# Performance work log

Hardware: AMD Instinct MI355X
Metric: run time of the kernel (lower is better)

Reference implementation:

```python
import jax, jax.numpy as jnp
import numpy as np

L, H, S, HID, E, TOPK = 2, 8, 1024, 512, 8, 2
FFN = 2 * HID
EPS = 1e-5


def setup_inputs() -> dict:
    key = jax.random.key(0)
    ks = jax.random.split(key, 20)
    B = 4
    sc = 0.02
    inp = {
        'x': jax.random.normal(ks[0], (B, S, HID), jnp.float32),
        'encoder_output': jax.random.normal(ks[1], (B, S, HID), jnp.float32),
        # two attentions per layer -> axis 1 of size 2 (0: masked self-attn, 1: cross-attn)
        'attn_wq': jax.random.normal(ks[2], (L, 2, HID, H * HID), jnp.float32) * sc,
        'attn_bq': jnp.zeros((L, 2, H * HID), jnp.float32),
        'attn_wk': jax.random.normal(ks[3], (L, 2, HID, H * HID), jnp.float32) * sc,
        'attn_bk': jnp.zeros((L, 2, H * HID), jnp.float32),
        'attn_wv': jax.random.normal(ks[4], (L, 2, HID, H * HID), jnp.float32) * sc,
        'attn_bv': jnp.zeros((L, 2, H * HID), jnp.float32),
        'attn_wo': jax.random.normal(ks[5], (L, 2, H * HID, HID), jnp.float32) * sc,
        'attn_bo': jnp.zeros((L, 2, HID), jnp.float32),
        'gate_w': jax.random.normal(ks[6], (L, HID, E), jnp.float32) * sc,
        'gate_b': jnp.zeros((L, E), jnp.float32),
        'exp_w1': jax.random.normal(ks[7], (L, E, HID, FFN), jnp.float32) * sc,
        'exp_b1': jnp.zeros((L, E, FFN), jnp.float32),
        'exp_w2': jax.random.normal(ks[8], (L, E, FFN, HID), jnp.float32) * sc,
        'exp_b2': jnp.zeros((L, E, HID), jnp.float32),
        'ln_g': jnp.ones((L, 3, HID), jnp.float32),
        'ln_b': jnp.zeros((L, 3, HID), jnp.float32),
    }
    return inp


def _layernorm(x, g, b):
    m = jnp.mean(x, -1, keepdims=True)
    v = jnp.mean(jnp.square(x - m), -1, keepdims=True)
    return g * (x - m) * jax.lax.rsqrt(v + EPS) + b


def _mha(q_in, k_in, v_in, wq, bq, wk, bk, wv, bv, wo, bo, masked):
    B = q_in.shape[0]
    # torch .view(-1, H, S, h) on [B, S, H*h]: raw memory reshape (faithful quirk)
    q = (q_in @ wq + bq).reshape(B, H, S, HID)
    k = (k_in @ wk + bk).reshape(B, H, S, HID)
    v = (v_in @ wv + bv).reshape(B, H, S, HID)
    scores = jnp.einsum('bhqd,bhkd->bhqk', q, k)  # d_k=1 -> scale = 1.0
    if masked:
        causal = jnp.triu(jnp.ones((S, S), jnp.float32), k=1)
        scores = jnp.where(causal == 1, -jnp.inf, scores)
    attn = jax.nn.softmax(scores, axis=-1)  # dropout off (eval)
    out = jnp.einsum('bhqk,bhkd->bhqd', attn, v)
    out = out.transpose(0, 2, 1, 3).reshape(B, S, H * HID)
    return out @ wo + bo


def _moe(x, gw, gb, w1, b1, w2, b2):
    gate = jax.nn.softmax(x @ gw + gb, axis=-1)  # [B,S,E]
    topw, topi = jax.lax.top_k(gate, TOPK)
    topw = topw / jnp.sum(topw, -1, keepdims=True)
    # faithful bug: the torch loop overwrites, so only k = TOPK-1 survives
    sel = topi[..., TOPK - 1]  # [B,S]
    wsel = topw[..., TOPK - 1]  # [B,S]
    y = jnp.zeros_like(x)
    for e in range(E):
        he = jax.nn.relu(x @ w1[e] + b1[e]) @ w2[e] + b2[e]
        y = y + jnp.where((sel == e)[..., None], he, 0.0)
    return y * wsel[..., None]


def reference(x, encoder_output, attn_wq, attn_bq, attn_wk, attn_bk, attn_wv,
              attn_bv, attn_wo, attn_bo, gate_w, gate_b, exp_w1, exp_b1,
              exp_w2, exp_b2, ln_g, ln_b):
    for l in range(L):
        a = _mha(x, x, x,
                 attn_wq[l, 0], attn_bq[l, 0], attn_wk[l, 0], attn_bk[l, 0],
                 attn_wv[l, 0], attn_bv[l, 0], attn_wo[l, 0], attn_bo[l, 0],
                 masked=True)
        x = _layernorm(a + x, ln_g[l, 0], ln_b[l, 0])
        # cross-attn: query & key from encoder, values from x (faithful to source)
        a2 = _mha(encoder_output, encoder_output, x,
                  attn_wq[l, 1], attn_bq[l, 1], attn_wk[l, 1], attn_bk[l, 1],
                  attn_wv[l, 1], attn_bv[l, 1], attn_wo[l, 1], attn_bo[l, 1],
                  masked=False)
        x = _layernorm(x + a2, ln_g[l, 1], ln_b[l, 1])
        f = _moe(x, gate_w[l], gate_b[l], exp_w1[l], exp_b1[l], exp_w2[l], exp_b2[l])
        x = _layernorm(x + f, ln_g[l, 2], ln_b[l, 2])
    return x
```

## Files before the change

kernel.cpp:

```cpp
#include <hip/hip_runtime.h>
#include <math.h>


typedef unsigned short bf16_t;
typedef __attribute__((ext_vector_type(8))) short s16x8;
typedef __attribute__((ext_vector_type(8))) unsigned short u16x8;
typedef __attribute__((ext_vector_type(4))) float f32x4;

__device__ __forceinline__ float bf2f(bf16_t u) {
    union { unsigned int i; float f; } v; v.i = ((unsigned int)u) << 16; return v.f;
}
__device__ __forceinline__ bf16_t f2bf(float f) {
    union { float f; unsigned int i; } v; v.f = f;
    unsigned int x = v.i;
    return (bf16_t)((x + 0x7fffu + ((x >> 16) & 1u)) >> 16);
}
__device__ __forceinline__ bf16_t bfhi_trunc(float x, float& rem) {
    union { float f; unsigned u; } v; v.f = x;
    unsigned hu = v.u & 0xFFFF0000u;
    union { unsigned u; float f; } h; h.u = hu;
    rem = x - h.f;
    return (bf16_t)(hu >> 16);
}
__device__ __forceinline__ void split_rne(float x, bf16_t& hi, bf16_t& lo) {
    bf16_t h = f2bf(x);
    float hf = bf2f(h);
    lo = f2bf(x - hf);
    hi = h;
}

__device__ __forceinline__ float waveReduceSum(float x) {
    x += __shfl_xor(x, 1);  x += __shfl_xor(x, 2);  x += __shfl_xor(x, 4);
    x += __shfl_xor(x, 8);  x += __shfl_xor(x, 16); x += __shfl_xor(x, 32);
    return x;
}
__device__ __forceinline__ float waveReduceMax(float x) {
    x = fmaxf(x, __shfl_xor(x, 1));  x = fmaxf(x, __shfl_xor(x, 2));
    x = fmaxf(x, __shfl_xor(x, 4));  x = fmaxf(x, __shfl_xor(x, 8));
    x = fmaxf(x, __shfl_xor(x, 16)); x = fmaxf(x, __shfl_xor(x, 32));
    return x;
}

__global__ void probe_kernel(const unsigned int* __restrict__ lng_u32,
                             int* __restrict__ flag)
{
    if (threadIdx.x == 0 && blockIdx.x == 0)
        *flag = (lng_u32[0] == 0x3F803F80u) ? 1 : 0;
}


__device__ __forceinline__ void stage_f32_row(const float* __restrict__ src,
                                              char* rowp, int h, int r)
{
    float xx[16];
    *(float4*)(xx + 0)  = *(const float4*)(src + 0);
    *(float4*)(xx + 4)  = *(const float4*)(src + 4);
    *(float4*)(xx + 8)  = *(const float4*)(src + 8);
    *(float4*)(xx + 12) = *(const float4*)(src + 12);
    u16x8 h0, h1, l0, l1;
#pragma unroll
    for (int i = 0; i < 8; i++) {
        float r0, r1;
        h0[i] = bfhi_trunc(xx[i], r0);      l0[i] = f2bf(r0);
        h1[i] = bfhi_trunc(xx[8 + i], r1);  l1[i] = f2bf(r1);
    }
    const int sw = (r & 7) << 4;
    *(u16x8*)(rowp + ((32 * h + 0)  ^ sw)) = h0;
    *(u16x8*)(rowp + ((32 * h + 16) ^ sw)) = h1;
    *(u16x8*)(rowp + ((64 + 32 * h + 0)  ^ sw)) = l0;
    *(u16x8*)(rowp + ((64 + 32 * h + 16) ^ sw)) = l1;
}

__device__ __forceinline__ void stage_bf16_row(const bf16_t* __restrict__ src,
                                               char* rowp, int h, int r)
{
    u16x8 v0 = *(const u16x8*)(src);
    u16x8 v1 = *(const u16x8*)(src + 8);
    const int sw = (r & 7) << 4;
    *(u16x8*)(rowp + ((32 * h + 0)  ^ sw)) = v0;
    *(u16x8*)(rowp + ((32 * h + 16) ^ sw)) = v1;
}

__device__ __forceinline__ void stage_pair_row(const bf16_t* __restrict__ hi,
                                               const bf16_t* __restrict__ lo,
                                               char* rowp, int h, int r)
{
    u16x8 h0 = *(const u16x8*)(hi);
    u16x8 h1 = *(const u16x8*)(hi + 8);
    u16x8 l0 = *(const u16x8*)(lo);
    u16x8 l1 = *(const u16x8*)(lo + 8);
    const int sw = (r & 7) << 4;
    *(u16x8*)(rowp + ((32 * h + 0)  ^ sw)) = h0;
    *(u16x8*)(rowp + ((32 * h + 16) ^ sw)) = h1;
    *(u16x8*)(rowp + ((64 + 32 * h + 0)  ^ sw)) = l0;
    *(u16x8*)(rowp + ((64 + 32 * h + 16) ^ sw)) = l1;
}

__device__ __forceinline__ void stage_wnn_f32(const float* __restrict__ src,
                                              int ldb, ushort (*Bs)[64],
                                              int kp2, int n8)
{
    float a0[8], a1[8];
    *(float4*)(a0 + 0) = *(const float4*)(src);
    *(float4*)(a0 + 4) = *(const float4*)(src + 4);
    *(float4*)(a1 + 0) = *(const float4*)(src + ldb);
    *(float4*)(a1 + 4) = *(const float4*)(src + ldb + 4);
#pragma unroll
    for (int j = 0; j < 8; j++) {
        int rr = n8 + j;
        float q0, q1;
        bf16_t h0 = bfhi_trunc(a0[j], q0);
        bf16_t h1 = bfhi_trunc(a1[j], q1);
        unsigned vh = (unsigned)h0 | ((unsigned)h1 << 16);
        unsigned vl = (unsigned)f2bf(q0) | ((unsigned)f2bf(q1) << 16);
        char* rp = (char*)&Bs[rr][0];
        int sw = (rr & 7) << 4;
        *(unsigned*)(rp + ((2 * kp2) ^ sw)) = vh;
        *(unsigned*)(rp + ((64 + 2 * kp2) ^ sw)) = vl;
    }
}

__device__ __forceinline__ void stage_wnn_bf16(const bf16_t* __restrict__ src,
                                               int ldb, ushort (*Bs)[64],
                                               int kp2, int n8, int base)
{
    u16x8 r0 = *(const u16x8*)(src);
    u16x8 r1 = *(const u16x8*)(src + ldb);
#pragma unroll
    for (int j = 0; j < 8; j++) {
        int rr = n8 + j;
        unsigned v = (unsigned)(unsigned short)r0[j] |
                     ((unsigned)(unsigned short)r1[j] << 16);
        *(unsigned*)((char*)&Bs[rr][0] + ((base + 2 * kp2) ^ ((rr & 7) << 4))) = v;
    }
}

template<bool NT, bool RELU, bool GATHER, bool SCALE, bool OUTP>
__device__ __forceinline__
void mgemm_body(int am, const float* __restrict__ aF,
                const bf16_t* __restrict__ aH, const bf16_t* __restrict__ aL,
                int bm, const float* __restrict__ bF,
                const bf16_t* __restrict__ bH, const bf16_t* __restrict__ bL,
                const float* __restrict__ biasF, const bf16_t* __restrict__ biasH,
                const bool bf, const bool hasb,
                float* __restrict__ Cp, bf16_t* __restrict__ CpH, long cplane,
                int lda, int ldb, int ldc,
                int Meff, const int* __restrict__ gl,
                const float* __restrict__ scalev,
                int kBeg, int kEnd, int m0, int n0)
{
    __shared__ __align__(16) ushort As[128][64];
    __shared__ __align__(16) ushort Bs[128][64];

    const int t   = threadIdx.x;
    const int sr  = t >> 1;
    const int sh  = t & 1;
    const int kp2 = (t & 15) * 2;
    const int n8  = (t >> 4) * 8;

    int agr = m0 + sr;
    if (GATHER) agr = gl[(m0 + sr < Meff) ? (m0 + sr) : (Meff - 1)];

    const int lane = t & 63;
    const int wv = t >> 6;
    const int wr = wv >> 1, wc = wv & 1;
    const int lr = lane & 15, kg = lane >> 4;

    int aoffH[4], aoffL[4], boffH[4], boffL[4];
#pragma unroll
    for (int i = 0; i < 4; i++) {
        int ra = wr * 64 + i * 16 + lr;
        int sa = (ra & 7) << 4;
        aoffH[i] = ra * 128 + ((kg * 16) ^ sa);
        aoffL[i] = ra * 128 + ((64 + kg * 16) ^ sa);
        int rb = wc * 64 + i * 16 + lr;
        int sb = (rb & 7) << 4;
        boffH[i] = rb * 128 + ((kg * 16) ^ sb);
        boffL[i] = rb * 128 + ((64 + kg * 16) ^ sb);
    }

    f32x4 acc[4][4];
#pragma unroll
    for (int i = 0; i < 4; i++)
#pragma unroll
        for (int j = 0; j < 4; j++)
            acc[i][j] = (f32x4){0.f, 0.f, 0.f, 0.f};

    const bool aHasLo = (am != 1);
    const bool bHasLo = (bm != 1);

    if (am >= 1 && bm >= 1) {
        u16x8 pa0, pa1, pa2, pa3;
        u16x8 pb0, pb1, pb2, pb3;

        auto loadT = [&](int k0) {
            long aoff = (long)agr * lda + k0 + sh * 16;
            pa0 = *(const u16x8*)(aH + aoff);
            pa1 = *(const u16x8*)(aH + aoff + 8);
            if (am == 2) {
                pa2 = *(const u16x8*)(aL + aoff);
                pa3 = *(const u16x8*)(aL + aoff + 8);
            }
            if (NT) {
                long boff = (long)(n0 + sr) * ldb + k0 + sh * 16;
                pb0 = *(const u16x8*)(bH + boff);
                pb1 = *(const u16x8*)(bH + boff + 8);
                if (bm == 2) {
                    pb2 = *(const u16x8*)(bL + boff);
                    pb3 = *(const u16x8*)(bL + boff + 8);
                }
            } else {
                long boff = (long)(k0 + kp2) * ldb + n0 + n8;
                pb0 = *(const u16x8*)(bH + boff);
                pb1 = *(const u16x8*)(bH + boff + ldb);
                if (bm == 2) {
                    pb2 = *(const u16x8*)(bL + boff);
                    pb3 = *(const u16x8*)(bL + boff + ldb);
                }
            }
        };
        auto storeT = [&]() {
            const int swA = (sr & 7) << 4;
            char* rowpA = (char*)&As[sr][0];
            *(u16x8*)(rowpA + ((32 * sh + 0)  ^ swA)) = pa0;
            *(u16x8*)(rowpA + ((32 * sh + 16) ^ swA)) = pa1;
            if (am == 2) {
                *(u16x8*)(rowpA + ((64 + 32 * sh + 0)  ^ swA)) = pa2;
                *(u16x8*)(rowpA + ((64 + 32 * sh + 16) ^ swA)) = pa3;
            }
            if (NT) {
                char* rowpB = (char*)&Bs[sr][0];
                *(u16x8*)(rowpB + ((32 * sh + 0)  ^ swA)) = pb0;
                *(u16x8*)(rowpB + ((32 * sh + 16) ^ swA)) = pb1;
                if (bm == 2) {
                    *(u16x8*)(rowpB + ((64 + 32 * sh + 0)  ^ swA)) = pb2;
                    *(u16x8*)(rowpB + ((64 + 32 * sh + 16) ^ swA)) = pb3;
                }
            } else {
#pragma unroll
                for (int j = 0; j < 8; j++) {
                    int rr = n8 + j;
                    int sw = (rr & 7) << 4;
                    char* rp = (char*)&Bs[rr][0];
                    unsigned vh = (unsigned)(unsigned short)pb0[j] |
                                  ((unsigned)(unsigned short)pb1[j] << 16);
                    *(unsigned*)(rp + ((2 * kp2) ^ sw)) = vh;
                    if (bm == 2) {
                        unsigned vl = (unsigned)(unsigned short)pb2[j] |
                                      ((unsigned)(unsigned short)pb3[j] << 16);
                        *(unsigned*)(rp + ((64 + 2 * kp2) ^ sw)) = vl;
                    }
                }
            }
        };

        loadT(kBeg);
        for (int k0 = kBeg; k0 < kEnd; k0 += 32) {
            __syncthreads();
            storeT();
            __syncthreads();
            if (k0 + 32 < kEnd) loadT(k0 + 32);

            s16x8 aHi[4], aLo[4];
#pragma unroll
            for (int i = 0; i < 4; i++)
                aHi[i] = *(const s16x8*)((const char*)As + aoffH[i]);
            if (aHasLo) {
#pragma unroll
                for (int i = 0; i < 4; i++)
                    aLo[i] = *(const s16x8*)((const char*)As + aoffL[i]);
            }
#pragma unroll
            for (int j = 0; j < 4; j++) {
                s16x8 bHi = *(const s16x8*)((const char*)Bs + boffH[j]);
#pragma unroll
                for (int i = 0; i < 4; i++)
                    acc[i][j] = __builtin_amdgcn_mfma_f32_16x16x32_bf16(
                        aHi[i], bHi, acc[i][j], 0, 0, 0);
                if (bHasLo) {
                    s16x8 bLo = *(const s16x8*)((const char*)Bs + boffL[j]);
#pragma unroll
                    for (int i = 0; i < 4; i++)
                        acc[i][j] = __builtin_amdgcn_mfma_f32_16x16x32_bf16(
                            aHi[i], bLo, acc[i][j], 0, 0, 0);
                }
                if (aHasLo) {
#pragma unroll
                    for (int i = 0; i < 4; i++)
                        acc[i][j] = __builtin_amdgcn_mfma_f32_16x16x32_bf16(
                            aLo[i], bHi, acc[i][j], 0, 0, 0);
                }
            }
        }
    } else {
        for (int k0 = kBeg; k0 < kEnd; k0 += 32) {
            __syncthreads();
            {
                char* rowp = (char*)&As[sr][0];
                long aoff = (long)agr * lda + k0 + sh * 16;
                if (am == 2)      stage_pair_row(aH + aoff, aL + aoff, rowp, sh, sr);
                else if (am == 1) stage_bf16_row(aH + aoff, rowp, sh, sr);
                else              stage_f32_row (aF + aoff, rowp, sh, sr);
            }
            if (NT) {
                char* rowp = (char*)&Bs[sr][0];
                long boff = (long)(n0 + sr) * ldb + k0 + sh * 16;
                if (bm == 2)      stage_pair_row(bH + boff, bL + boff, rowp, sh, sr);
                else if (bm == 1) stage_bf16_row(bH + boff, rowp, sh, sr);
                else              stage_f32_row (bF + boff, rowp, sh, sr);
            } else {
                long boff = (long)(k0 + kp2) * ldb + n0 + n8;
                if (bm == 2) {
                    stage_wnn_bf16(bH + boff, ldb, Bs, kp2, n8, 0);
                    stage_wnn_bf16(bL + boff, ldb, Bs, kp2, n8, 64);
                } else if (bm == 1) {
                    stage_wnn_bf16(bH + boff, ldb, Bs, kp2, n8, 0);
                } else {
                    stage_wnn_f32 (bF + boff, ldb, Bs, kp2, n8);
                }
            }
            __syncthreads();

            s16x8 aHi[4], aLo[4];
#pragma unroll
            for (int i = 0; i < 4; i++)
                aHi[i] = *(const s16x8*)((const char*)As + aoffH[i]);
            if (aHasLo) {
#pragma unroll
                for (int i = 0; i < 4; i++)
                    aLo[i] = *(const s16x8*)((const char*)As + aoffL[i]);
            }
#pragma unroll
            for (int j = 0; j < 4; j++) {
                s16x8 bHi = *(const s16x8*)((const char*)Bs + boffH[j]);
#pragma unroll
                for (int i = 0; i < 4; i++)
                    acc[i][j] = __builtin_amdgcn_mfma_f32_16x16x32_bf16(
                        aHi[i], bHi, acc[i][j], 0, 0, 0);
                if (bHasLo) {
                    s16x8 bLo = *(const s16x8*)((const char*)Bs + boffL[j]);
#pragma unroll
                    for (int i = 0; i < 4; i++)
                        acc[i][j] = __builtin_amdgcn_mfma_f32_16x16x32_bf16(
                            aHi[i], bLo, acc[i][j], 0, 0, 0);
                }
                if (aHasLo) {
#pragma unroll
                    for (int i = 0; i < 4; i++)
                        acc[i][j] = __builtin_amdgcn_mfma_f32_16x16x32_bf16(
                            aLo[i], bHi, acc[i][j], 0, 0, 0);
                }
            }
        }
    }

#pragma unroll
    for (int j = 0; j < 4; j++) {
        int col = n0 + wc * 64 + j * 16 + lr;
        float bv = 0.f;
        if (hasb) bv = bf ? bf2f(biasH[col]) : biasF[col];
#pragma unroll
        for (int i = 0; i < 4; i++) {
#pragma unroll
            for (int rr = 0; rr < 4; rr++) {
                int grow = m0 + wr * 64 + i * 16 + kg * 4 + rr;
                if (GATHER && grow >= Meff) continue;
                int crow = GATHER ? gl[grow] : grow;
                float v = acc[i][j][rr] + bv;
                if (RELU) v = fmaxf(v, 0.f);
                if (SCALE) v *= scalev[crow];
                if (OUTP) {
                    bf16_t hh, ll;
                    split_rne(v, hh, ll);
                    long off = (long)crow * ldc + col;
                    CpH[off] = hh;
                    CpH[cplane + off] = ll;
                } else {
                    Cp[(long)crow * ldc + col] = v;
                }
            }
        }
    }
}

template<bool NT, bool RELU, bool GATHER, bool SCALE,
         bool MASK_TRI, bool MASK_K, bool SPLITK, bool OUTP>
__global__ __launch_bounds__(256, 2)
void mgemm_kernel(int amode, int bmode,
                  const void* a32, const void* a16, const void* a16lo,
                  const void* b32, const void* b16, const void* b16lo,
                  const void* bias32, const void* bias16,
                  float* C, void* CH, long cplane,
                  int M, int N, int K, int lda, int ldb, int ldc,
                  long aZ, long bZ, long biasZ, long cZ,
                  const int* __restrict__ glist, const int* __restrict__ counts,
                  const float* __restrict__ scalev,
                  const int* __restrict__ dtf)
{
    if (MASK_TRI && blockIdx.x > blockIdx.y) return;
    const int e  = SPLITK ? 0 : blockIdx.z;
    const int n0 = blockIdx.x * 128, m0 = blockIdx.y * 128;
    int Meff = M;
    const int* gl = nullptr;
    if (GATHER) {
        gl = glist + e * 4096;
        Meff = counts[e];
        if (m0 >= Meff) return;
    }
    const bool bf = (*dtf != 0);
    const int am = (amode < 0) ? (bf ? 1 : 0) : amode;
    const int bm = (bmode < 0) ? (bf ? 1 : 0) : bmode;

    const float*  aF = (const float*)a32 + (long)e * aZ;
    const bf16_t* aH = (const bf16_t*)a16 + (long)e * aZ;
    const bf16_t* aL = (const bf16_t*)a16lo + (long)e * aZ;
    const long bOff  = SPLITK ? 0 : (long)e * bZ;
    const float*  bF = (const float*)b32 + bOff;
    const bf16_t* bH = (const bf16_t*)b16 + bOff;
    const bf16_t* bL = (const bf16_t*)b16lo + bOff;

    float* Cp = nullptr;
    bf16_t* CpH = nullptr;
    int kBeg = 0, kEnd = K;
    if (SPLITK) {
        const int kc  = blockIdx.z;
        const int kch = (int)bZ;
        kBeg = kc * kch;
        kEnd = kBeg + kch;
        Cp = C + (long)kc * cZ;
    } else {
        if (C)  Cp  = C + (long)e * cZ;
        if (CH) CpH = (bf16_t*)CH + (long)e * cZ;
        if (MASK_K) kEnd = (blockIdx.y + 1) * 128;
    }
    const bool hasb = !SPLITK && ((bias32 != nullptr) || (bias16 != nullptr));
    const float*  biasF = (const float*)bias32 + (long)e * biasZ;
    const bf16_t* biasH = (const bf16_t*)bias16 + (long)e * biasZ;

    mgemm_body<NT, RELU, GATHER, SCALE, OUTP>(am, aF, aH, aL, bm, bF, bH, bL,
        biasF, biasH, bf, hasb, Cp, CpH, cplane, lda, ldb, ldc, Meff, gl,
        scalev, kBeg, kEnd, m0, n0);
}

struct TriArgs {
    const void* aF[3]; const void* aH[3]; const void* aL[3];
    const void* w32[3]; const void* w16[3];
    const void* b32[3]; const void* b16[3];
    void* dstH[3];
    int am[3];
};

__global__ __launch_bounds__(256, 2)
void mgemm_tri_kernel(TriArgs ta, const int* __restrict__ dtf)
{
    const int z = blockIdx.z;
    const bool bf = (*dtf != 0);
    const int am = (ta.am[z] < 0) ? (bf ? 1 : 0) : ta.am[z];
    const int bm = bf ? 1 : 0;
    mgemm_body<false, false, false, false, true>(
        am, (const float*)ta.aF[z], (const bf16_t*)ta.aH[z], (const bf16_t*)ta.aL[z],
        bm, (const float*)ta.w32[z], (const bf16_t*)ta.w16[z], nullptr,
        (const float*)ta.b32[z], (const bf16_t*)ta.b16[z],
        bf, true,
        nullptr, (bf16_t*)ta.dstH[z], 4194304L,
        512, 4096, 4096,
        0, nullptr, nullptr,
        0, 512, blockIdx.y * 128, blockIdx.x * 128);
}

template<int NCH>
__global__ __launch_bounds__(256)
void reduce_kernel(const float* __restrict__ part,
                   const void* bias32, const void* bias16,
                   float* __restrict__ out, const int* __restrict__ dtf)
{
    const bool bf = (*dtf != 0);
    const int i = (blockIdx.x * 256 + threadIdx.x) * 4;
    float4 s = *(const float4*)(part + i);
#pragma unroll
    for (int c = 1; c < NCH; c++) {
        float4 p = *(const float4*)(part + (long)c * 524288 + i);
        s.x += p.x; s.y += p.y; s.z += p.z; s.w += p.w;
    }
    const int col = i & 511;
    float b0, b1, b2, b3;
    if (bf) {
        const bf16_t* bb = (const bf16_t*)bias16;
        b0 = bf2f(bb[col]); b1 = bf2f(bb[col + 1]);
        b2 = bf2f(bb[col + 2]); b3 = bf2f(bb[col + 3]);
    } else {
        const float* bb = (const float*)bias32;
        b0 = bb[col]; b1 = bb[col + 1]; b2 = bb[col + 2]; b3 = bb[col + 3];
    }
    out[i + 0] = s.x + b0; out[i + 1] = s.y + b1;
    out[i + 2] = s.z + b2; out[i + 3] = s.w + b3;
}

template<bool MASKED>
__global__ __launch_bounds__(256)
void softmax_kernel(float* __restrict__ sb)
{
    const int g = blockIdx.x * 4 + (threadIdx.x >> 6);
    const int lane = threadIdx.x & 63;
    const int r = g & 1023;
    float* row = sb + (long)g * 1024;
    bf16_t* rowh = (bf16_t*)row;
    const int n = MASKED ? (r + 1) : 1024;

    float vv[16];
    float m = -1e30f;
#pragma unroll
    for (int j = 0; j < 4; j++) {
        float4 v4 = *(const float4*)(row + j * 256 + lane * 4);
        const float* pv = (const float*)&v4;
#pragma unroll
        for (int c = 0; c < 4; c++) {
            int idx = j * 256 + lane * 4 + c;
            float x = (idx < n) ? pv[c] : -1e30f;
            vv[j * 4 + c] = x;
            m = fmaxf(m, x);
        }
    }
    m = waveReduceMax(m);
    float sum = 0.0f;
#pragma unroll
    for (int i = 0; i < 16; i++) {
        vv[i] = __expf(vv[i] - m);
        sum += vv[i];
    }
    sum = waveReduceSum(sum);
    float inv = 1.0f / sum;
#pragma unroll
    for (int j = 0; j < 4; j++) {
        ushort4 hh, ll;
        float p0 = vv[j * 4 + 0] * inv, p1 = vv[j * 4 + 1] * inv;
        float p2 = vv[j * 4 + 2] * inv, p3 = vv[j * 4 + 3] * inv;
        bf16_t h, l;
        split_rne(p0, h, l); hh.x = h; ll.x = l;
        split_rne(p1, h, l); hh.y = h; ll.y = l;
        split_rne(p2, h, l); hh.z = h; ll.z = l;
        split_rne(p3, h, l); hh.w = h; ll.w = l;
        *(ushort4*)(rowh + (j * 256 + lane * 4)) = hh;
        *(ushort4*)(rowh + 1024 + (j * 256 + lane * 4)) = ll;
    }
}

template<bool MASKED>
__global__ __launch_bounds__(256)
void flash_kernel(const bf16_t* __restrict__ qh, const bf16_t* __restrict__ ql,
                  const bf16_t* __restrict__ kh, const bf16_t* __restrict__ kl,
// ... 184 lines not shown
    if (lane == 0) {
        float m1 = -1e30f, m2 = -1e30f;
        int i1 = 0, i2 = 0;
#pragma unroll
        for (int e = 0; e < 8; e++) {
            float vv = logits[e];
            if (vv > m1) { m2 = m1; i2 = i1; m1 = vv; i1 = e; }
            else if (vv > m2) { m2 = vv; i2 = e; }
        }
        float ed = __expf(m2 - m1);
        sel[token]  = i2;
        wsel[token] = ed / (1.0f + ed);
    }
}

__global__ void zero_counts_kernel(int* __restrict__ counts)
{
    if (threadIdx.x < 8) counts[threadIdx.x] = 0;
}

__global__ __launch_bounds__(256)
void route_kernel(const int* __restrict__ sel, int* __restrict__ counts,
                  int* __restrict__ idx)
{
    int tk = blockIdx.x * 256 + threadIdx.x;
    int e = sel[tk] & 7;
    int pos = atomicAdd(&counts[e], 1) & 4095;
    idx[e * 4096 + pos] = tk;
}

extern "C" void kernel_launch(void* const* d_in, const int* in_sizes, int n_in,
                              void* d_out, int out_size, void* d_ws, size_t ws_size,
                              hipStream_t stream)
{
    const char* x_in = (const char*)d_in[0];
    const char* enc  = (const char*)d_in[1];
    const char* wq   = (const char*)d_in[2];
    const char* bq   = (const char*)d_in[3];
    const char* wk   = (const char*)d_in[4];
    const char* bk   = (const char*)d_in[5];
    const char* wv   = (const char*)d_in[6];
    const char* bv   = (const char*)d_in[7];
    const char* wo   = (const char*)d_in[8];
    const char* bo   = (const char*)d_in[9];
    const char* gw   = (const char*)d_in[10];
    const char* gb   = (const char*)d_in[11];
    const char* ew1  = (const char*)d_in[12];
    const char* eb1  = (const char*)d_in[13];
    const char* ew2  = (const char*)d_in[14];
    const char* eb2  = (const char*)d_in[15];
    const char* lng  = (const char*)d_in[16];
    const char* lnb  = (const char*)d_in[17];

    float* ws = (float*)d_ws;
    const long SZ_X = 4096L * 512;
    const long SZ_B = 1024L * 4096;
    float* xb = ws;
    float* ab = xb + SZ_X;
    float* qb = ab + SZ_X;
    float* kb = qb + SZ_B;
    float* vb = kb + SZ_B;
    float* cb = vb + SZ_B;
    float* h1 = qb;
    float* yb = kb;
    float* wselp = cb + SZ_B;
    int* selp   = (int*)(wselp + 4096);
    int* counts = selp + 4096;
    int* idxl   = counts + 8;
    int* dtf    = idxl + 8 * 4096;
    long sb_off = (((long)(dtf + 1 - (int*)ws)) + 3) & ~3L;
    float* sbuf = ws + sb_off;
    const long NEED = (sb_off + 8L * 1048576L) * 4L;
    const bool big = (ws_size >= (size_t)NEED);

    bf16_t* xh  = (bf16_t*)xb;   bf16_t* xl  = xh + 2097152;
    bf16_t* qh  = (bf16_t*)qb;   bf16_t* ql  = qh + 4194304;
    bf16_t* kh  = (bf16_t*)kb;   bf16_t* kl  = kh + 4194304;
    bf16_t* vh  = (bf16_t*)vb;   bf16_t* vl  = vh + 4194304;
    bf16_t* cbh = (bf16_t*)cb;   bf16_t* cbl = cbh + 4194304;
    bf16_t* h1h = (bf16_t*)h1;   bf16_t* h1l = h1h + 4194304;
    bf16_t* sbh = (bf16_t*)sbuf;

    dim3 blk(256);
    const long SB = 1024L * 512;
    const long L3 = 512L * 4096;
    const long LO = 4096L * 512;

    probe_kernel<<<1, 64, 0, stream>>>((const unsigned int*)lng, dtf);

    const char* cur = x_in;
    bool cur_is_ws = false;

    for (int l = 0; l < 2; l++) {
        for (int att = 0; att < 2; att++) {
            const long woff = (long)(l * 2 + att);
            const void* Wx32[4] = { wq + woff * L3 * 4, wk + woff * L3 * 4,
                                    wv + woff * L3 * 4, wo + woff * LO * 4 };
            const void* Wx16[4] = { wq + woff * L3 * 2, wk + woff * L3 * 2,
                                    wv + woff * L3 * 2, wo + woff * LO * 2 };
            const void* Bx32[4] = { bq + woff * 4096 * 4, bk + woff * 4096 * 4,
                                    bv + woff * 4096 * 4, bo + woff * 512 * 4 };
            const void* Bx16[4] = { bq + woff * 4096 * 2, bk + woff * 4096 * 2,
                                    bv + woff * 4096 * 2, bo + woff * 512 * 2 };

            for (int b = 0; b < 4; b++) {
                const bool aqk_in = (att == 1) || !cur_is_ws;
                void* dst3[3] = { qb, kb, vb };

                TriArgs ta;
                for (int m = 0; m < 3; m++) {
                    const bool a_in = (m == 2) ? !cur_is_ws : aqk_in;
                    if (a_in) {
                        const char* Asrc = (m == 2) ? x_in : ((att == 1) ? enc : x_in);
                        ta.am[m] = -1;
                        ta.aF[m] = Asrc + b * SB * 4;
                        ta.aH[m] = Asrc + b * SB * 2;
                        ta.aL[m] = nullptr;
                    } else {
                        ta.am[m] = 2;
                        ta.aF[m] = nullptr;
                        ta.aH[m] = xh + b * SB;
                        ta.aL[m] = xl + b * SB;
                    }
                    ta.w32[m] = Wx32[m]; ta.w16[m] = Wx16[m];
                    ta.b32[m] = Bx32[m]; ta.b16[m] = Bx16[m];
                    ta.dstH[m] = dst3[m];
                }
                mgemm_tri_kernel<<<dim3(32, 8, 3), blk, 0, stream>>>(ta, dtf);

                if (big) {
                    if (att == 0) {
                        mgemm_kernel<true, false, false, false, true, false, false, false>
                            <<<dim3(8, 8, 8), blk, 0, stream>>>(
                            2, 2, nullptr, qh, ql, nullptr, kh, kl,
                            nullptr, nullptr, sbuf, nullptr, 0,
                            1024, 1024, 512, 512, 512, 1024,
                            524288L, 524288L, 0, 1048576L,
                            nullptr, nullptr, nullptr, dtf);
                        softmax_kernel<true><<<2048, blk, 0, stream>>>(sbuf);
                        mgemm_kernel<false, false, false, false, false, true, false, true>
                            <<<dim3(4, 8, 8), blk, 0, stream>>>(
                            2, 2, nullptr, sbh, sbh + 1024, nullptr, vh, vl,
                            nullptr, nullptr, nullptr, cbh, 4194304L,
                            1024, 512, 1024, 2048, 512, 4096,
                            2097152L, 524288L, 0, 512L,
                            nullptr, nullptr, nullptr, dtf);
                    } else {
                        mgemm_kernel<true, false, false, false, false, false, false, false>
                            <<<dim3(8, 8, 8), blk, 0, stream>>>(
                            2, 2, nullptr, qh, ql, nullptr, kh, kl,
                            nullptr, nullptr, sbuf, nullptr, 0,
                            1024, 1024, 512, 512, 512, 1024,
                            524288L, 524288L, 0, 1048576L,
                            nullptr, nullptr, nullptr, dtf);
                        softmax_kernel<false><<<2048, blk, 0, stream>>>(sbuf);
                        mgemm_kernel<false, false, false, false, false, false, false, true>
                            <<<dim3(4, 8, 8), blk, 0, stream>>>(
                            2, 2, nullptr, sbh, sbh + 1024, nullptr, vh, vl,
                            nullptr, nullptr, nullptr, cbh, 4194304L,
                            1024, 512, 1024, 2048, 512, 4096,
                            2097152L, 524288L, 0, 512L,
                            nullptr, nullptr, nullptr, dtf);
                    }
                    mgemm_kernel<false, false, false, false, false, false, true, false>
                        <<<dim3(4, 8, 16), blk, 0, stream>>>(
                        2, -1, nullptr, cbh, cbl, Wx32[3], Wx16[3], nullptr,
                        nullptr, nullptr, sbuf, nullptr, 0,
                        1024, 512, 4096, 4096, 512, 512,
                        0, 256 , 0, 524288L ,
                        nullptr, nullptr, nullptr, dtf);
                    reduce_kernel<16><<<512, blk, 0, stream>>>(
                        sbuf, Bx32[3], Bx16[3], ab + b * SB, dtf);
                } else {
                    if (att == 0)
                        flash_kernel<true><<<dim3(32, 8), blk, 0, stream>>>(
                            qh, ql, kh, kl, vh, vl, cbh);
                    else
                        flash_kernel<false><<<dim3(32, 8), blk, 0, stream>>>(
                            qh, ql, kh, kl, vh, vl, cbh);
                    mgemm_kernel<false, false, false, false, false, false, false, false>
                        <<<dim3(4, 8, 1), blk, 0, stream>>>(
                        2, -1, nullptr, cbh, cbl, Wx32[3], Wx16[3], nullptr,
                        Bx32[3], Bx16[3], ab + b * SB, nullptr, 0,
                        1024, 512, 4096, 4096, 512, 512,
                        0, 0, 0, 0, nullptr, nullptr, nullptr, dtf);
                }
            }

            const void* G32  = lng + (long)(l * 3 + att) * 512 * 4;
            const void* G16  = lng + (long)(l * 3 + att) * 512 * 2;
            const void* Bt32 = lnb + (long)(l * 3 + att) * 512 * 4;
            const void* Bt16 = lnb + (long)(l * 3 + att) * 512 * 2;
            if (cur_is_ws)
                add_ln_kernel<1, 1><<<4096, blk, 0, stream>>>(
                    ab, nullptr, xh, xl, G32, G16, Bt32, Bt16, xh, xl, dtf);
            else
                add_ln_kernel<0, 1><<<4096, blk, 0, stream>>>(
                    ab, (const void*)cur, (const void*)cur, nullptr,
                    G32, G16, Bt32, Bt16, xh, xl, dtf);
            cur = (const char*)xb; cur_is_ws = true;
        }

        gate_kernel<<<1024, blk, 0, stream>>>(
            xh, xl, gw + (long)l * 512 * 8 * 4, gw + (long)l * 512 * 8 * 2,
            gb + (long)l * 8 * 4, gb + (long)l * 8 * 2, selp, wselp, dtf);
        zero_counts_kernel<<<1, 64, 0, stream>>>(counts);
        route_kernel<<<16, blk, 0, stream>>>(selp, counts, idxl);

        mgemm_kernel<false, true, true, false, false, false, false, true>
            <<<dim3(8, 32, 8), blk, 0, stream>>>(
            2, -1, nullptr, xh, xl,
            ew1 + (long)l * 8 * 512 * 1024 * 4, ew1 + (long)l * 8 * 512 * 1024 * 2,
            nullptr,
            eb1 + (long)l * 8 * 1024 * 4, eb1 + (long)l * 8 * 1024 * 2,
            nullptr, h1h, 4194304L,
            4096, 1024, 512, 512, 1024, 1024,
            0, 512L * 1024, 1024, 0, idxl, counts, nullptr, dtf);
        mgemm_kernel<false, false, true, true, false, false, false, false>
            <<<dim3(4, 32, 8), blk, 0, stream>>>(
            2, -1, nullptr, h1h, h1l,
            ew2 + (long)l * 8 * 1024 * 512 * 4, ew2 + (long)l * 8 * 1024 * 512 * 2,
            nullptr,
            eb2 + (long)l * 8 * 512 * 4, eb2 + (long)l * 8 * 512 * 2,
            yb, nullptr, 0,
            4096, 512, 1024, 1024, 512, 512,
            0, 1024L * 512, 512, 0, idxl, counts, wselp, dtf);

        const void* G32  = lng + (long)(l * 3 + 2) * 512 * 4;
        const void* G16  = lng + (long)(l * 3 + 2) * 512 * 2;
        const void* Bt32 = lnb + (long)(l * 3 + 2) * 512 * 4;
        const void* Bt16 = lnb + (long)(l * 3 + 2) * 512 * 2;
        if (l == 0)
            add_ln_kernel<1, 1><<<4096, blk, 0, stream>>>(
                yb, nullptr, xh, xl, G32, G16, Bt32, Bt16, xh, xl, dtf);
        else
            add_ln_kernel<1, 0><<<4096, blk, 0, stream>>>(
                yb, nullptr, xh, xl, G32, G16, Bt32, Bt16, d_out, nullptr, dtf);
    }
}
```

Baseline: 3.938 ms.

## Shrink GEMM tiles to 64x64 with single-wave 64-thread blocks

Reworks the shared split-bf16 MFMA GEMM from 128x128 tiles with four waves per block to 64x64 tiles computed by one 64-thread wave. Each thread now stages a full 32-wide K row, and all launch grids are scaled up accordingly. The aim is more blocks and better CU occupancy for the smaller and gathered MoE GEMMs. The cost is less data reuse per tile, which means more global memory traffic, and more staging work per thread.

```diff
diff --git a/kernel.cpp b/kernel.cpp
--- a/kernel.cpp
+++ b/kernel.cpp
@@ -49,65 +49,83 @@
 }
 
 
-__device__ __forceinline__ void stage_f32_row(const float* __restrict__ src,
-                                              char* rowp, int h, int r)
-{
-    float xx[16];
-    *(float4*)(xx + 0)  = *(const float4*)(src + 0);
-    *(float4*)(xx + 4)  = *(const float4*)(src + 4);
-    *(float4*)(xx + 8)  = *(const float4*)(src + 8);
-    *(float4*)(xx + 12) = *(const float4*)(src + 12);
-    u16x8 h0, h1, l0, l1;
-#pragma unroll
-    for (int i = 0; i < 8; i++) {
-        float r0, r1;
-        h0[i] = bfhi_trunc(xx[i], r0);      l0[i] = f2bf(r0);
-        h1[i] = bfhi_trunc(xx[8 + i], r1);  l1[i] = f2bf(r1);
-    }
+__device__ __forceinline__ void stage_row64_f32(const float* __restrict__ src,
+                                                char* rowp, int r)
+{
+    float xx[32];
+#pragma unroll
+    for (int c = 0; c < 8; c++)
+        *(float4*)(xx + c * 4) = *(const float4*)(src + c * 4);
     const int sw = (r & 7) << 4;
-    *(u16x8*)(rowp + ((32 * h + 0)  ^ sw)) = h0;
-    *(u16x8*)(rowp + ((32 * h + 16) ^ sw)) = h1;
-    *(u16x8*)(rowp + ((64 + 32 * h + 0)  ^ sw)) = l0;
-    *(u16x8*)(rowp + ((64 + 32 * h + 16) ^ sw)) = l1;
-}
-
-__device__ __forceinline__ void stage_bf16_row(const bf16_t* __restrict__ src,
-                                               char* rowp, int h, int r)
-{
-    u16x8 v0 = *(const u16x8*)(src);
-    u16x8 v1 = *(const u16x8*)(src + 8);
+#pragma unroll
+    for (int c = 0; c < 4; c++) {
+        u16x8 h, l;
+#pragma unroll
+        for (int i = 0; i < 8; i++) {
+            float rem;
+            h[i] = bfhi_trunc(xx[c * 8 + i], rem);
+            l[i] = f2bf(rem);
+        }
+        *(u16x8*)(rowp + ((c * 16) ^ sw)) = h;
+        *(u16x8*)(rowp + ((64 + c * 16) ^ sw)) = l;
+    }
+}
+
+__device__ __forceinline__ void stage_row64_bf16(const bf16_t* __restrict__ src,
+                                                 char* rowp, int r)
+{
     const int sw = (r & 7) << 4;
-    *(u16x8*)(rowp + ((32 * h + 0)  ^ sw)) = v0;
-    *(u16x8*)(rowp + ((32 * h + 16) ^ sw)) = v1;
-}
-
-__device__ __forceinline__ void stage_pair_row(const bf16_t* __restrict__ hi,
-                                               const bf16_t* __restrict__ lo,
-                                               char* rowp, int h, int r)
-{
-    u16x8 h0 = *(const u16x8*)(hi);
-    u16x8 h1 = *(const u16x8*)(hi + 8);
-    u16x8 l0 = *(const u16x8*)(lo);
-    u16x8 l1 = *(const u16x8*)(lo + 8);
+#pragma unroll
+    for (int c = 0; c < 4; c++)
+        *(u16x8*)(rowp + ((c * 16) ^ sw)) = *(const u16x8*)(src + c * 8);
+}
+
+__device__ __forceinline__ void stage_row64_pair(const bf16_t* __restrict__ hi,
+                                                 const bf16_t* __restrict__ lo,
+                                                 char* rowp, int r)
+{
     const int sw = (r & 7) << 4;
-    *(u16x8*)(rowp + ((32 * h + 0)  ^ sw)) = h0;
-    *(u16x8*)(rowp + ((32 * h + 16) ^ sw)) = h1;
-    *(u16x8*)(rowp + ((64 + 32 * h + 0)  ^ sw)) = l0;
-    *(u16x8*)(rowp + ((64 + 32 * h + 16) ^ sw)) = l1;
-}
-
-__device__ __forceinline__ void stage_wnn_f32(const float* __restrict__ src,
-                                              int ldb, ushort (*Bs)[64],
-                                              int kp2, int n8)
-{
-    float a0[8], a1[8];
-    *(float4*)(a0 + 0) = *(const float4*)(src);
-    *(float4*)(a0 + 4) = *(const float4*)(src + 4);
-    *(float4*)(a1 + 0) = *(const float4*)(src + ldb);
-    *(float4*)(a1 + 4) = *(const float4*)(src + ldb + 4);
+#pragma unroll
+    for (int c = 0; c < 4; c++) {
+        *(u16x8*)(rowp + ((c * 16) ^ sw)) = *(const u16x8*)(hi + c * 8);
+        *(u16x8*)(rowp + ((64 + c * 16) ^ sw)) = *(const u16x8*)(lo + c * 8);
+    }
+}
+
+__device__ __forceinline__ void stage_wnn64_bf16(const bf16_t* __restrict__ src,
+                                                 int ldb, ushort (*Bs)[64],
+                                                 int kp, int nc, int base)
+{
+    u16x8 r0a = *(const u16x8*)(src);
+    u16x8 r0b = *(const u16x8*)(src + 8);
+    u16x8 r1a = *(const u16x8*)(src + ldb);
+    u16x8 r1b = *(const u16x8*)(src + ldb + 8);
 #pragma unroll
     for (int j = 0; j < 8; j++) {
-        int rr = n8 + j;
+        int rr = nc + j;
+        unsigned v = (unsigned)(unsigned short)r0a[j] |
+                     ((unsigned)(unsigned short)r1a[j] << 16);
+        *(unsigned*)((char*)&Bs[rr][0] + ((base + 2 * kp) ^ ((rr & 7) << 4))) = v;
+        int rr2 = nc + 8 + j;
+        unsigned v2 = (unsigned)(unsigned short)r0b[j] |
+                      ((unsigned)(unsigned short)r1b[j] << 16);
+        *(unsigned*)((char*)&Bs[rr2][0] + ((base + 2 * kp) ^ ((rr2 & 7) << 4))) = v2;
+    }
+}
+
+__device__ __forceinline__ void stage_wnn64_f32(const float* __restrict__ src,
+                                                int ldb, ushort (*Bs)[64],
+                                                int kp, int nc)
+{
+    float a0[16], a1[16];
+#pragma unroll
+    for (int c = 0; c < 4; c++) {
+        *(float4*)(a0 + c * 4) = *(const float4*)(src + c * 4);
+        *(float4*)(a1 + c * 4) = *(const float4*)(src + ldb + c * 4);
+    }
+#pragma unroll
+    for (int j = 0; j < 16; j++) {
+        int rr = nc + j;
         float q0, q1;
         bf16_t h0 = bfhi_trunc(a0[j], q0);
         bf16_t h1 = bfhi_trunc(a1[j], q1);
@@ -115,23 +133,8 @@
         unsigned vl = (unsigned)f2bf(q0) | ((unsigned)f2bf(q1) << 16);
         char* rp = (char*)&Bs[rr][0];
         int sw = (rr & 7) << 4;
-        *(unsigned*)(rp + ((2 * kp2) ^ sw)) = vh;
-        *(unsigned*)(rp + ((64 + 2 * kp2) ^ sw)) = vl;
-    }
-}
-
-__device__ __forceinline__ void stage_wnn_bf16(const bf16_t* __restrict__ src,
-                                               int ldb, ushort (*Bs)[64],
-                                               int kp2, int n8, int base)
-{
-    u16x8 r0 = *(const u16x8*)(src);
-    u16x8 r1 = *(const u16x8*)(src + ldb);
-#pragma unroll
-    for (int j = 0; j < 8; j++) {
-        int rr = n8 + j;
-        unsigned v = (unsigned)(unsigned short)r0[j] |
-                     ((unsigned)(unsigned short)r1[j] << 16);
-        *(unsigned*)((char*)&Bs[rr][0] + ((base + 2 * kp2) ^ ((rr & 7) << 4))) = v;
+        *(unsigned*)(rp + ((2 * kp) ^ sw)) = vh;
+        *(unsigned*)(rp + ((64 + 2 * kp) ^ sw)) = vl;
     }
 }
 
@@ -149,34 +152,25 @@
                 const float* __restrict__ scalev,
                 int kBeg, int kEnd, int m0, int n0)
 {
-    __shared__ __align__(16) ushort As[128][64];
-    __shared__ __align__(16) ushort Bs[128][64];
-
-    const int t   = threadIdx.x;
-    const int sr  = t >> 1;
-    const int sh  = t & 1;
-    const int kp2 = (t & 15) * 2;
-    const int n8  = (t >> 4) * 8;
-
-    int agr = m0 + sr;
-    if (GATHER) agr = gl[(m0 + sr < Meff) ? (m0 + sr) : (Meff - 1)];
-
-    const int lane = t & 63;
-    const int wv = t >> 6;
-    const int wr = wv >> 1, wc = wv & 1;
-    const int lr = lane & 15, kg = lane >> 4;
-
-    int aoffH[4], aoffL[4], boffH[4], boffL[4];
+    __shared__ __align__(16) ushort As[64][64];
+    __shared__ __align__(16) ushort Bs[64][64];
+
+    const int t = threadIdx.x;
+    const int lr = t & 15, kg = t >> 4;
+
+    int agr = m0 + t;
+    if (GATHER) agr = gl[(m0 + t < Meff) ? (m0 + t) : (Meff - 1)];
+
+    const int kp = (t & 15) * 2;
+    const int nc = (t >> 4) * 16;
+
+    int offH[4], offL[4];
 #pragma unroll
     for (int i = 0; i < 4; i++) {
-        int ra = wr * 64 + i * 16 + lr;
+        int ra = i * 16 + lr;
         int sa = (ra & 7) << 4;
-        aoffH[i] = ra * 128 + ((kg * 16) ^ sa);
-        aoffL[i] = ra * 128 + ((64 + kg * 16) ^ sa);
-        int rb = wc * 64 + i * 16 + lr;
-        int sb = (rb & 7) << 4;
-        boffH[i] = rb * 128 + ((kg * 16) ^ sb);
-        boffL[i] = rb * 128 + ((64 + kg * 16) ^ sb);
+        offH[i] = ra * 128 + ((kg * 16) ^ sa);
+        offL[i] = ra * 128 + ((64 + kg * 16) ^ sa);
     }
 
     f32x4 acc[4][4];
@@ -190,65 +184,90 @@
     const bool bHasLo = (bm != 1);
 
     if (am >= 1 && bm >= 1) {
-        u16x8 pa0, pa1, pa2, pa3;
-        u16x8 pb0, pb1, pb2, pb3;
+        u16x8 pa0, pa1, pa2, pa3, pa4, pa5, pa6, pa7;
+        u16x8 pb0, pb1, pb2, pb3, pb4, pb5, pb6, pb7;
 
         auto loadT = [&](int k0) {
-            long aoff = (long)agr * lda + k0 + sh * 16;
+            long aoff = (long)agr * lda + k0;
             pa0 = *(const u16x8*)(aH + aoff);
             pa1 = *(const u16x8*)(aH + aoff + 8);
+            pa2 = *(const u16x8*)(aH + aoff + 16);
+            pa3 = *(const u16x8*)(aH + aoff + 24);
             if (am == 2) {
-                pa2 = *(const u16x8*)(aL + aoff);
-                pa3 = *(const u16x8*)(aL + aoff + 8);
+                pa4 = *(const u16x8*)(aL + aoff);
+                pa5 = *(const u16x8*)(aL + aoff + 8);
+                pa6 = *(const u16x8*)(aL + aoff + 16);
+                pa7 = *(const u16x8*)(aL + aoff + 24);
             }
             if (NT) {
-                long boff = (long)(n0 + sr) * ldb + k0 + sh * 16;
+                long boff = (long)(n0 + t) * ldb + k0;
                 pb0 = *(const u16x8*)(bH + boff);
                 pb1 = *(const u16x8*)(bH + boff + 8);
+                pb2 = *(const u16x8*)(bH + boff + 16);
+                pb3 = *(const u16x8*)(bH + boff + 24);
                 if (bm == 2) {
-                    pb2 = *(const u16x8*)(bL + boff);
-                    pb3 = *(const u16x8*)(bL + boff + 8);
+                    pb4 = *(const u16x8*)(bL + boff);
+                    pb5 = *(const u16x8*)(bL + boff + 8);
+                    pb6 = *(const u16x8*)(bL + boff + 16);
+                    pb7 = *(const u16x8*)(bL + boff + 24);
                 }
             } else {
-                long boff = (long)(k0 + kp2) * ldb + n0 + n8;
+                long boff = (long)(k0 + kp) * ldb + n0 + nc;
                 pb0 = *(const u16x8*)(bH + boff);
-                pb1 = *(const u16x8*)(bH + boff + ldb);
+                pb1 = *(const u16x8*)(bH + boff + 8);
+                pb2 = *(const u16x8*)(bH + boff + ldb);
+                pb3 = *(const u16x8*)(bH + boff + ldb + 8);
                 if (bm == 2) {
-                    pb2 = *(const u16x8*)(bL + boff);
-                    pb3 = *(const u16x8*)(bL + boff + ldb);
+                    pb4 = *(const u16x8*)(bL + boff);
+                    pb5 = *(const u16x8*)(bL + boff + 8);
+                    pb6 = *(const u16x8*)(bL + boff + ldb);
+                    pb7 = *(const u16x8*)(bL + boff + ldb + 8);
                 }
             }
         };
         auto storeT = [&]() {
-            const int swA = (sr & 7) << 4;
-            char* rowpA = (char*)&As[sr][0];
-            *(u16x8*)(rowpA + ((32 * sh + 0)  ^ swA)) = pa0;
-            *(u16x8*)(rowpA + ((32 * sh + 16) ^ swA)) = pa1;
+            const int sw = (t & 7) << 4;
+            char* ra_ = (char*)&As[t][0];
+            *(u16x8*)(ra_ + ((0)  ^ sw)) = pa0;
+            *(u16x8*)(ra_ + ((16) ^ sw)) = pa1;
+            *(u16x8*)(ra_ + ((32) ^ sw)) = pa2;
+            *(u16x8*)(ra_ + ((48) ^ sw)) = pa3;
             if (am == 2) {
-                *(u16x8*)(rowpA + ((64 + 32 * sh + 0)  ^ swA)) = pa2;
-                *(u16x8*)(rowpA + ((64 + 32 * sh + 16) ^ swA)) = pa3;
+                *(u16x8*)(ra_ + ((64)  ^ sw)) = pa4;
+                *(u16x8*)(ra_ + ((80)  ^ sw)) = pa5;
+                *(u16x8*)(ra_ + ((96)  ^ sw)) = pa6;
+                *(u16x8*)(ra_ + ((112) ^ sw)) = pa7;
             }
             if (NT) {
-                char* rowpB = (char*)&Bs[sr][0];
-                *(u16x8*)(rowpB + ((32 * sh + 0)  ^ swA)) = pb0;
-                *(u16x8*)(rowpB + ((32 * sh + 16) ^ swA)) = pb1;
+                char* rb_ = (char*)&Bs[t][0];
+                *(u16x8*)(rb_ + ((0)  ^ sw)) = pb0;
+                *(u16x8*)(rb_ + ((16) ^ sw)) = pb1;
+                *(u16x8*)(rb_ + ((32) ^ sw)) = pb2;
+                *(u16x8*)(rb_ + ((48) ^ sw)) = pb3;
                 if (bm == 2) {
-                    *(u16x8*)(rowpB + ((64 + 32 * sh + 0)  ^ swA)) = pb2;
-                    *(u16x8*)(rowpB + ((64 + 32 * sh + 16) ^ swA)) = pb3;
+                    *(u16x8*)(rb_ + ((64)  ^ sw)) = pb4;
+                    *(u16x8*)(rb_ + ((80)  ^ sw)) = pb5;
+                    *(u16x8*)(rb_ + ((96)  ^ sw)) = pb6;
+                    *(u16x8*)(rb_ + ((112) ^ sw)) = pb7;
                 }
             } else {
 #pragma unroll
                 for (int j = 0; j < 8; j++) {
-                    int rr = n8 + j;
-                    int sw = (rr & 7) << 4;
-                    char* rp = (char*)&Bs[rr][0];
-                    unsigned vh = (unsigned)(unsigned short)pb0[j] |
-                                  ((unsigned)(unsigned short)pb1[j] << 16);
-                    *(unsigned*)(rp + ((2 * kp2) ^ sw)) = vh;
+                    int rr = nc + j;
+                    unsigned v = (unsigned)(unsigned short)pb0[j] |
+                                 ((unsigned)(unsigned short)pb2[j] << 16);
+                    *(unsigned*)((char*)&Bs[rr][0] + ((2 * kp) ^ ((rr & 7) << 4))) = v;
+                    int rr2 = nc + 8 + j;
+                    unsigned v2 = (unsigned)(unsigned short)pb1[j] |
+                                  ((unsigned)(unsigned short)pb3[j] << 16);
+                    *(unsigned*)((char*)&Bs[rr2][0] + ((2 * kp) ^ ((rr2 & 7) << 4))) = v2;
                     if (bm == 2) {
-                        unsigned vl = (unsigned)(unsigned short)pb2[j] |
-                                      ((unsigned)(unsigned short)pb3[j] << 16);
-                        *(unsigned*)(rp + ((64 + 2 * kp2) ^ sw)) = vl;
+                        unsigned w = (unsigned)(unsigned short)pb4[j] |
+                                     ((unsigned)(unsigned short)pb6[j] << 16);
+                        *(unsigned*)((char*)&Bs[rr][0] + ((64 + 2 * kp) ^ ((rr & 7) << 4))) = w;
+                        unsigned w2 = (unsigned)(unsigned short)pb5[j] |
+                                      ((unsigned)(unsigned short)pb7[j] << 16);
+                        *(unsigned*)((char*)&Bs[rr2][0] + ((64 + 2 * kp) ^ ((rr2 & 7) << 4))) = w2;
                     }
                 }
             }
@@ -264,21 +283,21 @@
             s16x8 aHi[4], aLo[4];
 #pragma unroll
             for (int i = 0; i < 4; i++)
-                aHi[i] = *(const s16x8*)((const char*)As + aoffH[i]);
+                aHi[i] = *(const s16x8*)((const char*)As + offH[i]);
             if (aHasLo) {
 #pragma unroll
                 for (int i = 0; i < 4; i++)
-                    aLo[i] = *(const s16x8*)((const char*)As + aoffL[i]);
+                    aLo[i] = *(const s16x8*)((const char*)As + offL[i]);
             }
 #pragma unroll
             for (int j = 0; j < 4; j++) {
-                s16x8 bHi = *(const s16x8*)((const char*)Bs + boffH[j]);
+                s16x8 bHi = *(const s16x8*)((const char*)Bs + offH[j]);
 #pragma unroll
                 for (int i = 0; i < 4; i++)
                     acc[i][j] = __builtin_amdgcn_mfma_f32_16x16x32_bf16(
                         aHi[i], bHi, acc[i][j], 0, 0, 0);
                 if (bHasLo) {
-                    s16x8 bLo = *(const s16x8*)((const char*)Bs + boffL[j]);
+                    s16x8 bLo = *(const s16x8*)((const char*)Bs + offL[j]);
 #pragma unroll
                     for (int i = 0; i < 4; i++)
                         acc[i][j] = __builtin_amdgcn_mfma_f32_16x16x32_bf16(
@@ -296,27 +315,27 @@
         for (int k0 = kBeg; k0 < kEnd; k0 += 32) {
             __syncthreads();
             {
-                char* rowp = (char*)&As[sr][0];
-                long aoff = (long)agr * lda + k0 + sh * 16;
-                if (am == 2)      stage_pair_row(aH + aoff, aL + aoff, rowp, sh, sr);
-                else if (am == 1) stage_bf16_row(aH + aoff, rowp, sh, sr);
-                else              stage_f32_row (aF + aoff, rowp, sh, sr);
+                char* rowp = (char*)&As[t][0];
+                long aoff = (long)agr * lda + k0;
+                if (am == 2)      stage_row64_pair(aH + aoff, aL + aoff, rowp, t);
+                else if (am == 1) stage_row64_bf16(aH + aoff, rowp, t);
+                else              stage_row64_f32 (aF + aoff, rowp, t);
             }
             if (NT) {
-                char* rowp = (char*)&Bs[sr][0];
-                long boff = (long)(n0 + sr) * ldb + k0 + sh * 16;
-                if (bm == 2)      stage_pair_row(bH + boff, bL + boff, rowp, sh, sr);
-                else if (bm == 1) stage_bf16_row(bH + boff, rowp, sh, sr);
-                else              stage_f32_row (bF + boff, rowp, sh, sr);
+                char* rowp = (char*)&Bs[t][0];
+                long boff = (long)(n0 + t) * ldb + k0;
+                if (bm == 2)      stage_row64_pair(bH + boff, bL + boff, rowp, t);
+                else if (bm == 1) stage_row64_bf16(bH + boff, rowp, t);
+                else              stage_row64_f32 (bF + boff, rowp, t);
             } else {
-                long boff = (long)(k0 + kp2) * ldb + n0 + n8;
+                long boff = (long)(k0 + kp) * ldb + n0 + nc;
                 if (bm == 2) {
-                    stage_wnn_bf16(bH + boff, ldb, Bs, kp2, n8, 0);
-                    stage_wnn_bf16(bL + boff, ldb, Bs, kp2, n8, 64);
+                    stage_wnn64_bf16(bH + boff, ldb, Bs, kp, nc, 0);
+                    stage_wnn64_bf16(bL + boff, ldb, Bs, kp, nc, 64);
                 } else if (bm == 1) {
-                    stage_wnn_bf16(bH + boff, ldb, Bs, kp2, n8, 0);
+                    stage_wnn64_bf16(bH + boff, ldb, Bs, kp, nc, 0);
                 } else {
-                    stage_wnn_f32 (bF + boff, ldb, Bs, kp2, n8);
+                    stage_wnn64_f32 (bF + boff, ldb, Bs, kp, nc);
                 }
             }
             __syncthreads();
@@ -324,21 +343,21 @@
             s16x8 aHi[4], aLo[4];
 #pragma unroll
             for (int i = 0; i < 4; i++)
-                aHi[i] = *(const s16x8*)((const char*)As + aoffH[i]);
+                aHi[i] = *(const s16x8*)((const char*)As + offH[i]);
             if (aHasLo) {
 #pragma unroll
                 for (int i = 0; i < 4; i++)
-                    aLo[i] = *(const s16x8*)((const char*)As + aoffL[i]);
+                    aLo[i] = *(const s16x8*)((const char*)As + offL[i]);
             }
 #pragma unroll
             for (int j = 0; j < 4; j++) {
-                s16x8 bHi = *(const s16x8*)((const char*)Bs + boffH[j]);
+                s16x8 bHi = *(const s16x8*)((const char*)Bs + offH[j]);
 #pragma unroll
                 for (int i = 0; i < 4; i++)
                     acc[i][j] = __builtin_amdgcn_mfma_f32_16x16x32_bf16(
                         aHi[i], bHi, acc[i][j], 0, 0, 0);
                 if (bHasLo) {
-                    s16x8 bLo = *(const s16x8*)((const char*)Bs + boffL[j]);
+                    s16x8 bLo = *(const s16x8*)((const char*)Bs + offL[j]);
 #pragma unroll
                     for (int i = 0; i < 4; i++)
                         acc[i][j] = __builtin_amdgcn_mfma_f32_16x16x32_bf16(
@@ -356,14 +375,14 @@
 
 #pragma unroll
     for (int j = 0; j < 4; j++) {
-        int col = n0 + wc * 64 + j * 16 + lr;
+        int col = n0 + j * 16 + lr;
         float bv = 0.f;
         if (hasb) bv = bf ? bf2f(biasH[col]) : biasF[col];
 #pragma unroll
         for (int i = 0; i < 4; i++) {
 #pragma unroll
             for (int rr = 0; rr < 4; rr++) {
-                int grow = m0 + wr * 64 + i * 16 + kg * 4 + rr;
+                int grow = m0 + i * 16 + kg * 4 + rr;
                 if (GATHER && grow >= Meff) continue;
                 int crow = GATHER ? gl[grow] : grow;
                 float v = acc[i][j][rr] + bv;
@@ -385,7 +404,7 @@
 
 template<bool NT, bool RELU, bool GATHER, bool SCALE,
          bool MASK_TRI, bool MASK_K, bool SPLITK, bool OUTP>
-__global__ __launch_bounds__(256, 2)
+__global__ __launch_bounds__(64, 2)
 void mgemm_kernel(int amode, int bmode,
                   const void* a32, const void* a16, const void* a16lo,
                   const void* b32, const void* b16, const void* b16lo,
@@ -399,7 +418,7 @@
 {
     if (MASK_TRI && blockIdx.x > blockIdx.y) return;
     const int e  = SPLITK ? 0 : blockIdx.z;
-    const int n0 = blockIdx.x * 128, m0 = blockIdx.y * 128;
+    const int n0 = blockIdx.x * 64, m0 = blockIdx.y * 64;
     int Meff = M;
     const int* gl = nullptr;
     if (GATHER) {
@@ -431,7 +450,7 @@
     } else {
         if (C)  Cp  = C + (long)e * cZ;
         if (CH) CpH = (bf16_t*)CH + (long)e * cZ;
-        if (MASK_K) kEnd = (blockIdx.y + 1) * 128;
+        if (MASK_K) kEnd = (blockIdx.y + 1) * 64;
     }
     const bool hasb = !SPLITK && ((bias32 != nullptr) || (bias16 != nullptr));
     const float*  biasF = (const float*)bias32 + (long)e * biasZ;
@@ -450,7 +469,7 @@
     int am[3];
 };
 
-__global__ __launch_bounds__(256, 2)
+__global__ __launch_bounds__(64, 2)
 void mgemm_tri_kernel(TriArgs ta, const int* __restrict__ dtf)
 {
     const int z = blockIdx.z;
@@ -465,7 +484,7 @@
         nullptr, (bf16_t*)ta.dstH[z], 4194304L,
         512, 4096, 4096,
         0, nullptr, nullptr,
-        0, 512, blockIdx.y * 128, blockIdx.x * 128);
+        0, 512, blockIdx.y * 64, blockIdx.x * 64);
 }
 
 template<int NCH>
@@ -816,6 +835,7 @@
     bf16_t* sbh = (bf16_t*)sbuf;
 
     dim3 blk(256);
+    dim3 blk64(64);
     const long SB = 1024L * 512;
     const long L3 = 512L * 4096;
     const long LO = 4096L * 512;
@@ -860,12 +880,12 @@
                     ta.b32[m] = Bx32[m]; ta.b16[m] = Bx16[m];
                     ta.dstH[m] = dst3[m];
                 }
-                mgemm_tri_kernel<<<dim3(32, 8, 3), blk, 0, stream>>>(ta, dtf);
+                mgemm_tri_kernel<<<dim3(64, 16, 3), blk64, 0, stream>>>(ta, dtf);
 
                 if (big) {
                     if (att == 0) {
                         mgemm_kernel<true, false, false, false, true, false, false, false>
-                            <<<dim3(8, 8, 8), blk, 0, stream>>>(
+                            <<<dim3(16, 16, 8), blk64, 0, stream>>>(
                             2, 2, nullptr, qh, ql, nullptr, kh, kl,
                             nullptr, nullptr, sbuf, nullptr, 0,
                             1024, 1024, 512, 512, 512, 1024,
@@ -873,7 +893,7 @@
                             nullptr, nullptr, nullptr, dtf);
                         softmax_kernel<true><<<2048, blk, 0, stream>>>(sbuf);
                         mgemm_kernel<false, false, false, false, false, true, false, true>
-                            <<<dim3(4, 8, 8), blk, 0, stream>>>(
+                            <<<dim3(8, 16, 8), blk64, 0, stream>>>(
                             2, 2, nullptr, sbh, sbh + 1024, nullptr, vh, vl,
                             nullptr, nullptr, nullptr, cbh, 4194304L,
                             1024, 512, 1024, 2048, 512, 4096,
@@ -881,7 +901,7 @@
                             nullptr, nullptr, nullptr, dtf);
                     } else {
                         mgemm_kernel<true, false, false, false, false, false, false, false>
-                            <<<dim3(8, 8, 8), blk, 0, stream>>>(
+                            <<<dim3(16, 16, 8), blk64, 0, stream>>>(
                             2, 2, nullptr, qh, ql, nullptr, kh, kl,
                             nullptr, nullptr, sbuf, nullptr, 0,
                             1024, 1024, 512, 512, 512, 1024,
@@ -889,7 +909,7 @@
                             nullptr, nullptr, nullptr, dtf);
                         softmax_kernel<false><<<2048, blk, 0, stream>>>(sbuf);
                         mgemm_kernel<false, false, false, false, false, false, false, true>
-                            <<<dim3(4, 8, 8), blk, 0, stream>>>(
+                            <<<dim3(8, 16, 8), blk64, 0, stream>>>(
                             2, 2, nullptr, sbh, sbh + 1024, nullptr, vh, vl,
                             nullptr, nullptr, nullptr, cbh, 4194304L,
                             1024, 512, 1024, 2048, 512, 4096,
@@ -897,7 +917,7 @@
                             nullptr, nullptr, nullptr, dtf);
                     }
                     mgemm_kernel<false, false, false, false, false, false, true, false>
-                        <<<dim3(4, 8, 16), blk, 0, stream>>>(
+                        <<<dim3(8, 16, 16), blk64, 0, stream>>>(
                         2, -1, nullptr, cbh, cbl, Wx32[3], Wx16[3], nullptr,
                         nullptr, nullptr, sbuf, nullptr, 0,
                         1024, 512, 4096, 4096, 512, 512,
@@ -913,7 +933,7 @@
                         flash_kernel<false><<<dim3(32, 8), blk, 0, stream>>>(
                             qh, ql, kh, kl, vh, vl, cbh);
                     mgemm_kernel<false, false, false, false, false, false, false, false>
-                        <<<dim3(4, 8, 1), blk, 0, stream>>>(
+                        <<<dim3(8, 16, 1), blk64, 0, stream>>>(
                         2, -1, nullptr, cbh, cbl, Wx32[3], Wx16[3], nullptr,
                         Bx32[3], Bx16[3], ab + b * SB, nullptr, 0,
                         1024, 512, 4096, 4096, 512, 512,
@@ -942,7 +962,7 @@
         route_kernel<<<16, blk, 0, stream>>>(selp, counts, idxl);
 
         mgemm_kernel<false, true, true, false, false, false, false, true>
-            <<<dim3(8, 32, 8), blk, 0, stream>>>(
+            <<<dim3(16, 64, 8), blk64, 0, stream>>>(
             2, -1, nullptr, xh, xl,
             ew1 + (long)l * 8 * 512 * 1024 * 4, ew1 + (long)l * 8 * 512 * 1024 * 2,
             nullptr,
@@ -951,7 +971,7 @@
             4096, 1024, 512, 512, 1024, 1024,
             0, 512L * 1024, 1024, 0, idxl, counts, nullptr, dtf);
         mgemm_kernel<false, false, true, true, false, false, false, false>
-            <<<dim3(4, 32, 8), blk, 0, stream>>>(
+            <<<dim3(8, 64, 8), blk64, 0, stream>>>(
             2, -1, nullptr, h1h, h1l,
             ew2 + (long)l * 8 * 1024 * 512 * 4, ew2 + (long)l * 8 * 1024 * 512 * 2,
             nullptr,
```

After: 5.977 ms. +51.8%, slower.
